# Performance work log

Hardware: AMD Instinct MI355X
Metric: run time of the kernel (lower is better)

The kernel has to match this reference:

```python
import jax, jax.numpy as jnp
import numpy as np

SQ = 1.0 / np.sqrt(2.0)

def _haar_filters():
    dec_lo = np.array([SQ, SQ], np.float32); dec_hi = np.array([-SQ, SQ], np.float32)
    rec_lo = np.array([SQ, SQ], np.float32); rec_hi = np.array([SQ, -SQ], np.float32)
    def bank(lo, hi):
        ks = []
        for fz in (lo, hi):
            for fy in (lo, hi):
                for fx in (lo, hi):
                    ks.append(np.einsum('i,j,k->ijk', fz, fy, fx))
        return jnp.asarray(np.stack(ks, 0))  # [8,2,2,2]
    return bank(dec_lo, dec_hi), bank(rec_lo, rec_hi)

WT_F, IWT_F = _haar_filters()

def dwt3(x):
    # stride-2 2x2x2 cross-correlation == reshape + einsum (kernel size == stride)
    B, C, D, H, W = x.shape
    xr = x.reshape(B, C, D // 2, 2, H // 2, 2, W // 2, 2)
    return jnp.einsum('bcdzhywx,fzyx->bcfdhw', xr, WT_F)  # [B,C,8,D/2,H/2,W/2]

def idwt3(x):
    # conv_transpose3d stride 2 kernel 2: no overlap -> einsum + reshape
    B, C, _, D, H, W = x.shape
    out = jnp.einsum('bcfdhw,fzyx->bcdzhywx', x, IWT_F)
    return out.reshape(B, C, 2 * D, 2 * H, 2 * W)

def dwconv3(x, w, b=None):
    # depthwise 3x3x3 conv, padding SAME (torch padding='same', groups=C)
    y = jax.lax.conv_general_dilated(
        x, w, (1, 1, 1), 'SAME',
        dimension_numbers=('NCDHW', 'OIDHW', 'NCDHW'),
        feature_group_count=x.shape[1])
    if b is not None:
        y = y + b[None, :, None, None, None]
    return y

WT_LEVELS = 2

def setup_inputs() -> dict:
    key = jax.random.key(0)
    ks = jax.random.split(key, 6)
    B, C, D, H, W = 1, 64, 64, 64, 64
    return {
        'x': jax.random.normal(ks[0], (B, C, D, H, W), jnp.float32),
        'base_w': jax.random.normal(ks[1], (C, 1, 3, 3, 3), jnp.float32) * 0.1,
        'base_b': jax.random.normal(ks[2], (C,), jnp.float32) * 0.02,
        'base_scale_w': jnp.ones((1, C, 1, 1, 1), jnp.float32),
        'wconv_w0': jax.random.normal(ks[3], (C * 8, 1, 3, 3, 3), jnp.float32) * 0.1,
        'wconv_w1': jax.random.normal(ks[4], (C * 8, 1, 3, 3, 3), jnp.float32) * 0.1,
        'wscale0': jnp.full((1, C * 8, 1, 1, 1), 0.1, jnp.float32),
        'wscale1': jnp.full((1, C * 8, 1, 1, 1), 0.1, jnp.float32),
        'lambd': jnp.float32(0.05),
    }

def reference(x, base_w, base_b, base_scale_w, wconv_w0, wconv_w1, wscale0, wscale1, lambd):
    wconv_ws = (wconv_w0, wconv_w1)
    wscales = (wscale0, wscale1)
    lls, hfs, shapes = [], [], []
    cur = x
    for i in range(WT_LEVELS):
        shapes.append(cur.shape)
        pd, ph, pw = cur.shape[2] % 2, cur.shape[3] % 2, cur.shape[4] % 2
        if pd or ph or pw:
            cur = jnp.pad(cur, ((0, 0), (0, 0), (0, pd), (0, ph), (0, pw)))
        cx = dwt3(cur)                     # [B,C,8,d,h,w]
        cur = cx[:, :, 0]                  # LL passes to next level
        B, C, _, d, h, w = cx.shape
        t = dwconv3(cx.reshape(B, C * 8, d, h, w), wconv_ws[i])
        t = t.reshape(B, C, 8, d, h, w)
        ll, hf = t[:, :, :1], t[:, :, 1:]
        hf = jnp.sign(hf) * jax.nn.relu(jnp.abs(hf) - lambd)  # soft threshold
        t = jnp.concatenate([ll, hf], axis=2)
        t = (t.reshape(B, C * 8, d, h, w) * wscales[i]).reshape(B, C, 8, d, h, w)
        lls.append(t[:, :, 0]); hfs.append(t[:, :, 1:])
    nxt = jnp.float32(0.0)
    for i in range(WT_LEVELS - 1, -1, -1):
        cll = lls[i] + nxt
        cx = jnp.concatenate([cll[:, :, None], hfs[i]], axis=2)
        nxt = idwt3(cx)
        sh = shapes[i]
        nxt = nxt[:, :, :sh[2], :sh[3], :sh[4]]
    base = dwconv3(x, base_w, base_b) * base_scale_w
    return base + nxt
```

## Files before the change

### kernel.cpp

```cpp
#include <hip/hip_runtime.h>

#define SQ3F 0.35355339059327379f

__device__ __forceinline__ float rfl(float v) {
    return __int_as_float(__builtin_amdgcn_readfirstlane(__float_as_int(v)));
}

__device__ __forceinline__ void haar_fwd(const float v[8], float o[8]) {
    float ax[8];
#pragma unroll
    for (int i = 0; i < 4; ++i) {
        float a = v[2 * i], b = v[2 * i + 1];
        ax[2 * i]     = a + b;
        ax[2 * i + 1] = b - a;
    }
    float ay[8];
#pragma unroll
    for (int z = 0; z < 2; ++z)
#pragma unroll
        for (int bx = 0; bx < 2; ++bx) {
            float a = ax[z * 4 + bx], b = ax[z * 4 + 2 + bx];
            ay[z * 4 + bx]     = a + b;
            ay[z * 4 + 2 + bx] = b - a;
        }
#pragma unroll
    for (int j = 0; j < 4; ++j) {
        float a = ay[j], b = ay[4 + j];
        o[j]     = (a + b) * SQ3F;
        o[4 + j] = (b - a) * SQ3F;
    }
}

__device__ __forceinline__ void haar_inv(const float t[8], float o[8]) {
    float az[8];
#pragma unroll
    for (int j = 0; j < 4; ++j) {
        float lo = t[j], hi = t[4 + j];
        az[j]     = lo + hi;
        az[4 + j] = lo - hi;
    }
    float ay[8];
#pragma unroll
    for (int z = 0; z < 2; ++z)
#pragma unroll
        for (int bx = 0; bx < 2; ++bx) {
            float lo = az[z * 4 + bx], hi = az[z * 4 + 2 + bx];
            ay[z * 4 + bx]     = lo + hi;
            ay[z * 4 + 2 + bx] = lo - hi;
        }
#pragma unroll
    for (int i = 0; i < 4; ++i) {
        float lo = ay[2 * i], hi = ay[2 * i + 1];
        o[2 * i]     = (lo + hi) * SQ3F;
        o[2 * i + 1] = (lo - hi) * SQ3F;
    }
}

__global__ __launch_bounds__(512, 6) void fused_l0_k(
    const float* __restrict__ x, const float* __restrict__ wt,
    const float* __restrict__ wscale, const float* __restrict__ lambd_p,
    float* __restrict__ t0, float* __restrict__ cx1) {
    __shared__ __align__(16) float pl[8][32][36];
    int bx   = ((blockIdx.x & 7) << 7) + (blockIdx.x >> 3);
    int slab = bx & 15;
    int c    = bx >> 4;
    int z0   = slab * 2;
    int tid  = threadIdx.x;

    {
        int fi   = tid >> 6;
        int rowi = (tid >> 1) & 31;
        pl[fi][rowi][(tid & 1) * 33] = 0.f;
    }

    int f    = __builtin_amdgcn_readfirstlane(tid >> 6);
    int lane = tid & 63;
    int cty  = lane >> 1;
    int cx0i = (lane & 1) * 16;
    int cc   = c * 8 + f;
    float wv[27];
    const float* wp = wt + cc * 27;
#pragma unroll
    for (int k = 0; k < 27; ++k) wv[k] = rfl(wp[k]);
    float lam = rfl(*lambd_p);
    float sc  = rfl(wscale[cc]);

    const float* xc = x + ((long)c << 18);

    float acc[2][16];
#pragma unroll
    for (int s = 0; s < 2; ++s)
#pragma unroll
        for (int j = 0; j < 16; ++j) acc[s][j] = 0.f;

    float llq00 = 0.f, llq01 = 0.f;

#pragma unroll
    for (int pp = 0; pp < 4; ++pp) {
        int p       = z0 - 1 + pp;
        bool pvalid = (p >= 0) && (p <= 31);
        __syncthreads();
        if (pvalid) {
            int cell = 2 * tid;
            int y    = cell >> 5;
            int xx   = cell & 31;
            float v0[8], v1[8];
#pragma unroll
            for (int z = 0; z < 2; ++z)
#pragma unroll
                for (int yy = 0; yy < 2; ++yy) {
                    float4 q = *(const float4*)(xc + (((2 * p + z) << 6) +
                                                      (2 * y + yy)) * 64 + 2 * xx);
                    v0[z * 4 + yy * 2]     = q.x;
                    v0[z * 4 + yy * 2 + 1] = q.y;
                    v1[z * 4 + yy * 2]     = q.z;
                    v1[z * 4 + yy * 2 + 1] = q.w;
                }
            float o0[8], o1[8];
            haar_fwd(v0, o0);
            haar_fwd(v1, o1);
#pragma unroll
            for (int k = 0; k < 8; ++k) {
                pl[k][y][xx + 1] = o0[k];
                pl[k][y][xx + 2] = o1[k];
            }
            if (pp == 1) {
                llq00 = o0[0];
                llq01 = o1[0];
            }
            if (pp == 2) {
                float l10 = o0[0], l11 = o1[0];
                float p00 = __shfl_xor(llq00, 16);
                float p01 = __shfl_xor(llq01, 16);
                float p10 = __shfl_xor(l10, 16);
                float p11 = __shfl_xor(l11, 16);
                int yp = (tid >> 4) & 1;
                float v[8];
                if (yp == 0) {
                    v[0] = llq00; v[1] = llq01; v[2] = p00; v[3] = p01;
                    v[4] = l10;   v[5] = l11;   v[6] = p10; v[7] = p11;
                } else {
                    v[0] = p00;   v[1] = p01;   v[2] = llq00; v[3] = llq01;
                    v[4] = p10;   v[5] = p11;   v[6] = l10;   v[7] = l11;
                }
                float o[8];
                haar_fwd(v, o);
                int d  = z0 >> 1;
                int hy = (tid >> 4) >> 1;
                int wx = tid & 15;
                int sA = (d * 16 + hy) * 16 + wx;
                int f0 = yp * 4;
#pragma unroll
                for (int q = 0; q < 4; ++q)
                    cx1[((c * 8 + f0 + q) << 12) + sA] = o[f0 + q];
            }
        }
        __syncthreads();
        if (pvalid) {
#pragma unroll
            for (int dy = 0; dy < 3; ++dy) {
                int yy = cty - 1 + dy;
                if ((unsigned)yy < 32u) {
                    float r[18];
                    {
                        const float* rp = &pl[f][yy][cx0i];
                        float4 a0 = *(const float4*)(rp);
                        float4 a1 = *(const float4*)(rp + 4);
                        float4 a2 = *(const float4*)(rp + 8);
                        float4 a3 = *(const float4*)(rp + 12);
                        float2 a4 = *(const float2*)(rp + 16);
                        r[0]  = a0.x; r[1]  = a0.y; r[2]  = a0.z; r[3]  = a0.w;
                        r[4]  = a1.x; r[5]  = a1.y; r[6]  = a1.z; r[7]  = a1.w;
                        r[8]  = a2.x; r[9]  = a2.y; r[10] = a2.z; r[11] = a2.w;
                        r[12] = a3.x; r[13] = a3.y; r[14] = a3.z; r[15] = a3.w;
                        r[16] = a4.x; r[17] = a4.y;
                    }
#pragma unroll
                    for (int dz = 0; dz < 3; ++dz) {
                        int rel = pp - dz;
                        if (rel >= 0 && rel <= 1) {
#pragma unroll
                            for (int dx = 0; dx < 3; ++dx) {
                                float wgt = wv[dz * 9 + dy * 3 + dx];
#pragma unroll
                                for (int j = 0; j < 16; ++j)
                                    acc[rel][j] += r[dx + j] * wgt;
                            }
                        }
                    }
                }
            }
        }
        {
            int rel = pp - 2;
            if (rel >= 0 && rel <= 1) {
                int zc = z0 + rel;
                float res[16];
#pragma unroll
                for (int j = 0; j < 16; ++j) {
                    float t = acc[rel][j];
                    if (f != 0) {
                        float a = fabsf(t) - lam;
                        t       = a > 0.f ? copysignf(a, t) : 0.f;
                    }
                    res[j]      = t * sc;
                    acc[rel][j] = 0.f;
                }
                float* op = t0 + ((long)cc << 15) + (zc << 10) + cty * 32 + cx0i;
#pragma unroll
                for (int q = 0; q < 4; ++q)
                    *(float4*)(op + q * 4) = float4{res[q * 4], res[q * 4 + 1],
                                                    res[q * 4 + 2], res[q * 4 + 3]};
            }
        }
    }
}

template <int S, int SLOT>
__device__ __forceinline__ void load_plane4(const float* __restrict__ ip,
                                            int z, int ty, int x0,
                                            float win[4][3][6]) {
    bool zok = ((unsigned)z < (unsigned)S);
    const float* pp = ip + z * S * S;
#pragma unroll
    for (int dy = 0; dy < 3; ++dy) {
        int yy  = ty - 1 + dy;
        bool yok = zok && ((unsigned)yy < (unsigned)S);
        const float* rp = pp + yy * S;
        win[SLOT][dy][0] = (yok && x0 > 0) ? rp[x0 - 1] : 0.f;
        float4 m = yok ? *(const float4*)(rp + x0) : float4{0.f, 0.f, 0.f, 0.f};
        win[SLOT][dy][1] = m.x;
        win[SLOT][dy][2] = m.y;
        win[SLOT][dy][3] = m.z;
        win[SLOT][dy][4] = m.w;
        win[SLOT][dy][5] = (yok && (x0 + 4 < S)) ? rp[x0 + 4] : 0.f;
    }
}

template <int S, int SP, int SC, int SN>
__device__ __forceinline__ void conv_compute(int zo, int ty, int x0,
                                             const float* __restrict__ wv,
                                             const float win[4][3][6], float lam,
                                             float sc, bool hf,
                                             float* __restrict__ op) {
    float acc[4] = {0.f, 0.f, 0.f, 0.f};
#pragma unroll
    for (int dy = 0; dy < 3; ++dy)
#pragma unroll
        for (int dx = 0; dx < 3; ++dx) {
            float w0 = wv[0 * 9 + dy * 3 + dx];
            float w1 = wv[1 * 9 + dy * 3 + dx];
            float w2 = wv[2 * 9 + dy * 3 + dx];
#pragma unroll
            for (int j = 0; j < 4; ++j) {
                acc[j] += win[SP][dy][dx + j] * w0;
                acc[j] += win[SC][dy][dx + j] * w1;
                acc[j] += win[SN][dy][dx + j] * w2;
            }
        }
    float4 r;
    float* rr = (float*)&r;
#pragma unroll
    for (int j = 0; j < 4; ++j) {
        float t = acc[j];
        if (hf) {
            float a = fabsf(t) - lam;
            t       = a > 0.f ? copysignf(a, t) : 0.f;
        }
        rr[j] = t * sc;
    }
    *(float4*)(op + (zo * S + ty) * S + x0) = r;
}

template <int S, int CPB>
__global__ __launch_bounds__(256) void dwconv_soft_pipe_k(
    const float* __restrict__ in, const float* __restrict__ wt,
    const float* __restrict__ wscale, const float* __restrict__ lambd_p,
    float* __restrict__ out) {
    constexpr int TX = S / 4;
    int bxl = ((blockIdx.x & 7) << 7) + (blockIdx.x >> 3);
    int tid = threadIdx.x;
    int tx  = tid % TX;
    int ty  = (tid / TX) % S;
    int cs  = tid / (TX * S);
    int zc  = bxl & 7;
    int cg  = bxl >> 3;
    int cc  = cg * CPB + cs;
    const float* ip = in + (long)cc * (S * S * S);
    float* op       = out + (long)cc * (S * S * S);
    float wv[27];
#pragma unroll
    for (int k = 0; k < 27; ++k) wv[k] = wt[cc * 27 + k];
    float lam = *lambd_p;
    float sc  = wscale[cc];
    bool hf   = (cc & 7) != 0;
    int x0    = 4 * tx;
    int z0    = 2 * zc;

    float win[4][3][6];
    if ((zc & 1) == 0) {
        load_plane4<S, 3>(ip, z0 - 1, ty, x0, win);
        load_plane4<S, 0>(ip, z0,     ty, x0, win);
        load_plane4<S, 1>(ip, z0 + 1, ty, x0, win);
        load_plane4<S, 2>(ip, z0 + 2, ty, x0, win);
        conv_compute<S, 3, 0, 1>(z0,     ty, x0, wv, win, lam, sc, hf, op);
        conv_compute<S, 0, 1, 2>(z0 + 1, ty, x0, wv, win, lam, sc, hf, op);
    } else {
        load_plane4<S, 1>(ip, z0 - 1, ty, x0, win);
        load_plane4<S, 2>(ip, z0,     ty, x0, win);
        load_plane4<S, 3>(ip, z0 + 1, ty, x0, win);
        load_plane4<S, 0>(ip, z0 + 2, ty, x0, win);
        conv_compute<S, 1, 2, 3>(z0,     ty, x0, wv, win, lam, sc, hf, op);
        conv_compute<S, 2, 3, 0>(z0 + 1, ty, x0, wv, win, lam, sc, hf, op);
    }
}

__global__ __launch_bounds__(256, 3) void final_k2(
    const float* __restrict__ x, const float* __restrict__ t0,
    const float* __restrict__ t1, const float* __restrict__ bw,
    const float* __restrict__ bb, const float* __restrict__ bscale,
    float* __restrict__ out) {
    __shared__ float xs[18 * 10 * 67];
    int bx = blockIdx.x;
    int c  = bx >> 5;
    int ti = bx & 31;
    int dt = ti >> 3;
    int ht = ti & 7;
    const float* xc = x + ((long)c << 18);

    int tid = threadIdx.x;
    int wc  = tid & 7;
    int hc  = (tid >> 3) & 3;
    int dc  = tid >> 5;
    int d   = dt * 8 + dc;
    int h   = ht * 4 + hc;
    int w0  = wc * 4;

    int cell0 = (d << 10) + (h << 5) + w0;
    float4 t0v[8];
#pragma unroll
    for (int f = 0; f < 8; ++f)
        t0v[f] = *(const float4*)(t0 + (((long)(c * 8 + f)) << 15) + cell0);
    int s1b = ((d >> 1) * 16 + (h >> 1)) * 16 + (w0 >> 1);
    float2 t1v[8];
#pragma unroll
    for (int f = 0; f < 8; ++f)
        t1v[f] = *(const float2*)(t1 + ((c * 8 + f) << 12) + s1b);

    int zg0 = 16 * dt - 1, yg0 = 8 * ht - 1;
    constexpr int TOT = 18 * 10 * 66;
#pragma unroll 1
    for (int k = 0; k < 10; ++k) {
        float v[5];
        int off[5];
#pragma unroll
        for (int b = 0; b < 5; ++b) {
            int i  = tid + (k * 5 + b) * 256;
            v[b]   = 0.f;
            off[b] = -1;
            if (i < TOT) {
                int pz = i / 660;
                int r  = i - pz * 660;
                int py = r / 66;
                int px = r - py * 66;
                int zg = zg0 + pz, yg = yg0 + py, xg = px - 1;
                bool ok = ((unsigned)zg < 64u) && ((unsigned)yg < 64u) &&
                          ((unsigned)xg < 64u);
                if (ok) v[b] = xc[(zg << 12) + (yg << 6) + xg];
                off[b] = (pz * 10 + py) * 67 + px;
            }
        }
#pragma unroll
        for (int b = 0; b < 5; ++b)
            if (off[b] >= 0) xs[off[b]] = v[b];
    }
    const float* wp0 = bw + c * 27;
    float wv[27];
#pragma unroll
    for (int k = 0; k < 27; ++k) wv[k] = wp0[k];
    float bias = bb[c], scl = bscale[c];
    __syncthreads();

    float acc[2][2][8];
#pragma unroll
    for (int oz = 0; oz < 2; ++oz)
#pragma unroll
        for (int oy = 0; oy < 2; ++oy)
#pragma unroll
            for (int m = 0; m < 8; ++m) acc[oz][oy][m] = 0.f;

#pragma unroll
    for (int pz = 0; pz < 4; ++pz) {
        float r[4][10];
#pragma unroll
        for (int py = 0; py < 4; ++py)
#pragma unroll
            for (int k = 0; k < 10; ++k)
                r[py][k] = xs[((2 * dc + pz) * 10 + (2 * hc + py)) * 67 + 8 * wc + k];
#pragma unroll
        for (int oz = 0; oz < 2; ++oz) {
            int kz = pz - oz;
            if (kz >= 0 && kz <= 2) {
#pragma unroll
                for (int py = 0; py < 4; ++py)
#pragma unroll
                    for (int oy = 0; oy < 2; ++oy) {
                        int ky = py - oy;
                        if (ky >= 0 && ky <= 2) {
#pragma unroll
                            for (int kx = 0; kx < 3; ++kx) {
                                float wgt = wv[kz * 9 + ky * 3 + kx];
#pragma unroll
                                for (int m = 0; m < 8; ++m)
                                    acc[oz][oy][m] += r[py][m + kx] * wgt;
                            }
                        }
                    }
            }
        }
    }

#pragma unroll
    for (int j = 0; j < 4; ++j) {
        int w = w0 + j;
        float tf[8];
#pragma unroll
        for (int f = 0; f < 8; ++f) tf[f] = ((const float*)&t0v[f])[j];
        float add = 0.f;
#pragma unroll
        for (int f = 0; f < 8; ++f) {
            float v  = (j >> 1) ? t1v[f].y : t1v[f].x;
            float sg = 1.f;
            if ((f & 4) && (d & 1)) sg = -sg;
            if ((f & 2) && (h & 1)) sg = -sg;
            if ((f & 1) && (j & 1)) sg = -sg;
            add += sg * v;
        }
        tf[0] += add * SQ3F;
        float contrib[8];
        haar_inv(tf, contrib);
#pragma unroll
        for (int oz = 0; oz < 2; ++oz)
#pragma unroll
            for (int oy = 0; oy < 2; ++oy) {
                float2 rr;
                rr.x = (acc[oz][oy][2 * j] + bias) * scl + contrib[oz * 4 + oy * 2];
                rr.y = (acc[oz][oy][2 * j + 1] + bias) * scl +
                       contrib[oz * 4 + oy * 2 + 1];
                *(float2*)(out + ((long)c << 18) + ((2 * d + oz) << 12) +
                           ((2 * h + oy) << 6) + 2 * w) = rr;
            }
    }
}

extern "C" void kernel_launch(void* const* d_in, const int* in_sizes, int n_in,
                              void* d_out, int out_size, void* d_ws, size_t ws_size,
                              hipStream_t stream) {
    const float* x      = (const float*)d_in[0];
    const float* base_w = (const float*)d_in[1];
    const float* base_b = (const float*)d_in[2];
    const float* base_s = (const float*)d_in[3];
    const float* w0     = (const float*)d_in[4];
    const float* w1     = (const float*)d_in[5];
    const float* ws0    = (const float*)d_in[6];
    const float* ws1    = (const float*)d_in[7];
    const float* lambd  = (const float*)d_in[8];
    float* out = (float*)d_out;

    float* t0  = (float*)d_ws;
    float* cx1 = t0 + 16777216;
    float* t1  = cx1 + 2097152;

    fused_l0_k<<<1024, 512, 0, stream>>>(x, w0, ws0, lambd, t0, cx1);
    dwconv_soft_pipe_k<16, 4><<<1024, 256, 0, stream>>>(cx1, w1, ws1, lambd, t1);
    final_k2<<<2048, 256, 0, stream>>>(x, t0, t1, base_w, base_b, base_s, out);
}
```

Baseline: 217.8 us.

## Double-buffer level-0 LDS planes and overlap global loads with depthwise conv

Restructures the fused level-0 kernel into a software pipeline with two LDS plane buffers. Each iteration first issues the global loads for the next Haar plane, then runs the 3x3x3 depthwise conv on the previously staged plane, then writes the new plane into the other buffer. This drops one __syncthreads per plane and hides global-load latency behind FMA work. In exchange it doubles shared memory and lowers the launch-bounds occupancy hint from 6 to 4 blocks.

```diff
diff --git a/kernel.cpp b/kernel.cpp
--- a/kernel.cpp
+++ b/kernel.cpp
@@ -56,11 +56,11 @@
     }
 }
 
-__global__ __launch_bounds__(512, 6) void fused_l0_k(
+__global__ __launch_bounds__(512, 4) void fused_l0_k(
     const float* __restrict__ x, const float* __restrict__ wt,
     const float* __restrict__ wscale, const float* __restrict__ lambd_p,
     float* __restrict__ t0, float* __restrict__ cx1) {
-    __shared__ __align__(16) float pl[8][32][36];
+    __shared__ __align__(16) float pl[2][8][32][36];
     int bx   = ((blockIdx.x & 7) << 7) + (blockIdx.x >> 3);
     int slab = bx & 15;
     int c    = bx >> 4;
@@ -70,7 +70,8 @@
     {
         int fi   = tid >> 6;
         int rowi = (tid >> 1) & 31;
-        pl[fi][rowi][(tid & 1) * 33] = 0.f;
+        pl[0][fi][rowi][(tid & 1) * 33] = 0.f;
+        pl[1][fi][rowi][(tid & 1) * 33] = 0.f;
     }
 
     int f    = __builtin_amdgcn_readfirstlane(tid >> 6);
@@ -87,6 +88,20 @@
 
     const float* xc = x + ((long)c << 18);
 
+    int cell = 2 * tid;
+    int y    = cell >> 5;
+    int xx   = cell & 31;
+
+    float4 pre[4];
+    auto issue_loads = [&](int p) {
+#pragma unroll
+        for (int z = 0; z < 2; ++z)
+#pragma unroll
+            for (int yy = 0; yy < 2; ++yy)
+                pre[z * 2 + yy] = *(const float4*)(
+                    xc + (((2 * p + z) << 6) + (2 * y + yy)) * 64 + 2 * xx);
+    };
+
     float acc[2][16];
 #pragma unroll
     for (int s = 0; s < 2; ++s)
@@ -96,21 +111,84 @@
     float llq00 = 0.f, llq01 = 0.f;
 
 #pragma unroll
-    for (int pp = 0; pp < 4; ++pp) {
-        int p       = z0 - 1 + pp;
-        bool pvalid = (p >= 0) && (p <= 31);
-        __syncthreads();
-        if (pvalid) {
-            int cell = 2 * tid;
-            int y    = cell >> 5;
-            int xx   = cell & 31;
+    for (int i = 0; i < 5; ++i) {
+        int p    = z0 - 1 + i;
+        bool sv  = (i < 4) && (p >= 0) && (p <= 31);
+        int pf   = z0 - 2 + i;
+        bool fv  = (i >= 1) && (pf >= 0) && (pf <= 31);
+
+        if (sv) {
+            issue_loads(p);
+            __builtin_amdgcn_sched_barrier(0);
+        }
+
+        if (fv) {
+            constexpr int dummy = 0; (void)dummy;
+#pragma unroll
+            for (int dy = 0; dy < 3; ++dy) {
+                int yy = cty - 1 + dy;
+                if ((unsigned)yy < 32u) {
+                    float r[18];
+                    {
+                        const float* rp = &pl[(i - 1) & 1][f][yy][cx0i];
+                        float4 a0 = *(const float4*)(rp);
+                        float4 a1 = *(const float4*)(rp + 4);
+                        float4 a2 = *(const float4*)(rp + 8);
+                        float4 a3 = *(const float4*)(rp + 12);
+                        float2 a4 = *(const float2*)(rp + 16);
+                        r[0]  = a0.x; r[1]  = a0.y; r[2]  = a0.z; r[3]  = a0.w;
+                        r[4]  = a1.x; r[5]  = a1.y; r[6]  = a1.z; r[7]  = a1.w;
+                        r[8]  = a2.x; r[9]  = a2.y; r[10] = a2.z; r[11] = a2.w;
+                        r[12] = a3.x; r[13] = a3.y; r[14] = a3.z; r[15] = a3.w;
+                        r[16] = a4.x; r[17] = a4.y;
+                    }
+#pragma unroll
+                    for (int dz = 0; dz < 3; ++dz) {
+                        int rel = (i - 1) - dz;
+                        if (rel >= 0 && rel <= 1) {
+#pragma unroll
+                            for (int dx = 0; dx < 3; ++dx) {
+                                float wgt = wv[dz * 9 + dy * 3 + dx];
+#pragma unroll
+                                for (int j = 0; j < 16; ++j)
+                                    acc[rel][j] += r[dx + j] * wgt;
+                            }
+                        }
+                    }
+                }
+            }
+        }
+
+        {
+            int rel = i - 3;
+            if (rel >= 0 && rel <= 1) {
+                int zc = z0 + rel;
+                float res[16];
+#pragma unroll
+                for (int j = 0; j < 16; ++j) {
+                    float t = acc[rel][j];
+                    if (f != 0) {
+                        float a = fabsf(t) - lam;
+                        t       = a > 0.f ? copysignf(a, t) : 0.f;
+                    }
+                    res[j]      = t * sc;
+                    acc[rel][j] = 0.f;
+                }
+                float* op = t0 + ((long)cc << 15) + (zc << 10) + cty * 32 + cx0i;
+#pragma unroll
+                for (int q = 0; q < 4; ++q)
+                    *(float4*)(op + q * 4) = float4{res[q * 4], res[q * 4 + 1],
+                                                    res[q * 4 + 2], res[q * 4 + 3]};
+            }
+        }
+
+        if (sv) {
             float v0[8], v1[8];
 #pragma unroll
             for (int z = 0; z < 2; ++z)
 #pragma unroll
                 for (int yy = 0; yy < 2; ++yy) {
-                    float4 q = *(const float4*)(xc + (((2 * p + z) << 6) +
-                                                      (2 * y + yy)) * 64 + 2 * xx);
+                    float4 q = pre[z * 2 + yy];
                     v0[z * 4 + yy * 2]     = q.x;
                     v0[z * 4 + yy * 2 + 1] = q.y;
                     v1[z * 4 + yy * 2]     = q.z;
@@ -121,14 +199,14 @@
             haar_fwd(v1, o1);
 #pragma unroll
             for (int k = 0; k < 8; ++k) {
-                pl[k][y][xx + 1] = o0[k];
-                pl[k][y][xx + 2] = o1[k];
-            }
-            if (pp == 1) {
+                pl[i & 1][k][y][xx + 1] = o0[k];
+                pl[i & 1][k][y][xx + 2] = o1[k];
+            }
+            if (i == 1) {
                 llq00 = o0[0];
                 llq01 = o1[0];
             }
-            if (pp == 2) {
+            if (i == 2) {
                 float l10 = o0[0], l11 = o1[0];
                 float p00 = __shfl_xor(llq00, 16);
                 float p01 = __shfl_xor(llq01, 16);
@@ -156,63 +234,6 @@
             }
         }
         __syncthreads();
-        if (pvalid) {
-#pragma unroll
-            for (int dy = 0; dy < 3; ++dy) {
-                int yy = cty - 1 + dy;
-                if ((unsigned)yy < 32u) {
-                    float r[18];
-                    {
-                        const float* rp = &pl[f][yy][cx0i];
-                        float4 a0 = *(const float4*)(rp);
-                        float4 a1 = *(const float4*)(rp + 4);
-                        float4 a2 = *(const float4*)(rp + 8);
-                        float4 a3 = *(const float4*)(rp + 12);
-                        float2 a4 = *(const float2*)(rp + 16);
-                        r[0]  = a0.x; r[1]  = a0.y; r[2]  = a0.z; r[3]  = a0.w;
-                        r[4]  = a1.x; r[5]  = a1.y; r[6]  = a1.z; r[7]  = a1.w;
-                        r[8]  = a2.x; r[9]  = a2.y; r[10] = a2.z; r[11] = a2.w;
-                        r[12] = a3.x; r[13] = a3.y; r[14] = a3.z; r[15] = a3.w;
-                        r[16] = a4.x; r[17] = a4.y;
-                    }
-#pragma unroll
-                    for (int dz = 0; dz < 3; ++dz) {
-                        int rel = pp - dz;
-                        if (rel >= 0 && rel <= 1) {
-#pragma unroll
-                            for (int dx = 0; dx < 3; ++dx) {
-                                float wgt = wv[dz * 9 + dy * 3 + dx];
-#pragma unroll
-                                for (int j = 0; j < 16; ++j)
-                                    acc[rel][j] += r[dx + j] * wgt;
-                            }
-                        }
-                    }
-                }
-            }
-        }
-        {
-            int rel = pp - 2;
-            if (rel >= 0 && rel <= 1) {
-                int zc = z0 + rel;
-                float res[16];
-#pragma unroll
-                for (int j = 0; j < 16; ++j) {
-                    float t = acc[rel][j];
-                    if (f != 0) {
-                        float a = fabsf(t) - lam;
-                        t       = a > 0.f ? copysignf(a, t) : 0.f;
-                    }
-                    res[j]      = t * sc;
-                    acc[rel][j] = 0.f;
-                }
-                float* op = t0 + ((long)cc << 15) + (zc << 10) + cty * 32 + cx0i;
-#pragma unroll
-                for (int q = 0; q < 4; ++q)
-                    *(float4*)(op + q * 4) = float4{res[q * 4], res[q * 4 + 1],
-                                                    res[q * 4 + 2], res[q * 4 + 3]};
-            }
-        }
     }
 }
 
```

Result: faster. 208.5 us (-4.3%).
